# Performance work log

Hardware: AMD Instinct MI355X
Metric: run time of the kernel (lower is better)

Reference implementation:

```python
import jax, jax.numpy as jnp
import numpy as np


def gcn_conv(x, src, dst, W, b, n_nodes):
    # PyG GCNConv default: add self-loops, symmetric normalization D^-1/2 A D^-1/2.
    h = x @ W  # [N, out]
    # degree with unit edge weights + self loop
    deg = jnp.zeros((n_nodes,), dtype=x.dtype).at[dst].add(1.0) + 1.0
    dinv = jax.lax.rsqrt(deg)  # deg >= 1, safe
    norm = dinv[src] * dinv[dst]  # [E]
    msg = h[src] * norm[:, None]  # [E, out] gather + scale
    out = jnp.zeros_like(h).at[dst].add(msg)  # scatter-add aggregate
    # self-loop contribution: norm_ii = dinv_i^2
    out = out + h * (dinv * dinv)[:, None]
    return out + b


def setup_inputs() -> dict:
    key = jax.random.key(0)
    ks = jax.random.split(key, 10)
    N, E, F_in, H, G = 100000, 1600000, 128, 128, 256
    x = jax.random.normal(ks[0], (N, F_in), dtype=jnp.float32)
    edge_index = jax.random.randint(ks[1], (2, E), 0, N, dtype=jnp.int64)
    batch = jnp.sort(jax.random.randint(ks[2], (N,), 0, G, dtype=jnp.int64))
    s1 = 1.0 / np.sqrt(F_in)
    s2 = 1.0 / np.sqrt(H)
    W1 = jax.random.uniform(ks[3], (F_in, H), jnp.float32, -s1, s1)
    b1 = jnp.zeros((H,), jnp.float32)
    W2 = jax.random.uniform(ks[4], (H, H), jnp.float32, -s2, s2)
    b2 = jnp.zeros((H,), jnp.float32)
    Wlin = jax.random.uniform(ks[5], (H, 2), jnp.float32, -s2, s2)
    blin = jax.random.uniform(ks[6], (2,), jnp.float32, -s2, s2)
    return {"x": x, "edge_index": edge_index, "batch": batch, "num_graphs": G,
            "W1": W1, "b1": b1, "W2": W2, "b2": b2, "Wlin": Wlin, "blin": blin}


def reference(x, edge_index, batch, num_graphs, W1, b1, W2, b2, Wlin, blin):
    n_nodes = x.shape[0]
    src, dst = edge_index[0], edge_index[1]
    h = jax.nn.relu(gcn_conv(x, src, dst, W1, b1, n_nodes))
    h = jax.nn.relu(gcn_conv(h, src, dst, W2, b2, n_nodes))
    # global_mean_pool over graphs
    sums = jax.ops.segment_sum(h, batch, num_segments=num_graphs)
    counts = jax.ops.segment_sum(jnp.ones((n_nodes,), h.dtype), batch, num_segments=num_graphs)
    pooled = sums / jnp.maximum(counts, 1.0)[:, None]  # [G, H]
    return pooled @ Wlin + blin  # [G, 2]
```

## Files before the change

### kernel.cpp

```cpp
#include <hip/hip_runtime.h>
#include <hip/hip_bf16.h>


#define FEAT 128
#define GRAPHS 256
#define CH 2048
#define BSH 8
#define MAXNB 512

typedef short bf16x8 __attribute__((ext_vector_type(8)));
typedef float f32x4 __attribute__((ext_vector_type(4)));

__device__ inline unsigned bf16rne(float f) {
    unsigned u = __float_as_uint(f);
    return (u + 0x7FFFu + ((u >> 16) & 1u)) >> 16;
}

#define SWZ(row, kbyte) ((kbyte) ^ (((row) & 7) << 4))

__global__ __launch_bounds__(256) void kb_hist(const int* __restrict__ dst, int E, int NB,
                                               int* __restrict__ bhist) {
    __shared__ int h[MAXNB];
    for (int i = threadIdx.x; i < NB; i += 256) h[i] = 0;
    __syncthreads();
    int stride = gridDim.x * 256;
    for (int i = blockIdx.x * 256 + threadIdx.x; i < E; i += stride)
        atomicAdd(&h[dst[i] >> BSH], 1);
    __syncthreads();
    for (int i = threadIdx.x; i < NB; i += 256)
        if (h[i]) atomicAdd(&bhist[i], h[i]);
}

__global__ void kb_scan(const int* __restrict__ bhist, int NB,
                        int* __restrict__ bbase, int* __restrict__ bcur) {
    __shared__ int s[512];
    int t = threadIdx.x;
    int v = (t < NB) ? bhist[t] : 0;
    s[t] = v;
    __syncthreads();
    for (int d = 1; d < 512; d <<= 1) {
        int a = (t >= d) ? s[t - d] : 0;
        __syncthreads();
        s[t] += a;
        __syncthreads();
    }
    if (t < NB) { int e = s[t] - v; bbase[t] = e; bcur[t] = e; }
}

__global__ __launch_bounds__(256) void kb_group(const int* __restrict__ src,
                                                const int* __restrict__ dst, int E, int NB,
                                                int* __restrict__ bcur,
                                                unsigned* __restrict__ stg) {
    __shared__ int lhist[MAXNB], lcur[MAXNB], gdelta[MAXNB], sc[512];
    __shared__ unsigned lpak[CH];
    __shared__ int gp[CH];
    int t = threadIdx.x;
    int base = blockIdx.x * CH;
    int n = E - base; if (n > CH) n = CH;

    for (int i = t; i < NB; i += 256) lhist[i] = 0;
    __syncthreads();

    unsigned pk[8]; int bk[8]; int nl = 0;
#pragma unroll
    for (int j = 0; j < 8; ++j) {
        int k = j * 256 + t;
        if (k < n) {
            int d = dst[base + k];
            int sv = src[base + k];
            int b = d >> BSH;
            pk[nl] = ((unsigned)(d & ((1 << BSH) - 1)) << 17) | (unsigned)sv;
            bk[nl] = b; nl++;
            atomicAdd(&lhist[b], 1);
        }
    }
    __syncthreads();

    for (int i = t; i < 512; i += 256) sc[i] = (i < NB) ? lhist[i] : 0;
    __syncthreads();
    for (int d = 1; d < 512; d <<= 1) {
        int a0 = (t >= d) ? sc[t - d] : 0;
        int a1 = sc[t + 256 - d];
        __syncthreads();
        sc[t] += a0; sc[t + 256] += a1;
        __syncthreads();
    }
    for (int i = t; i < NB; i += 256) {
        int c = lhist[i];
        int lb = sc[i] - c;
        lcur[i] = lb;
        int g = c ? atomicAdd(&bcur[i], c) : 0;
        gdelta[i] = g - lb;
    }
    __syncthreads();

    for (int j = 0; j < nl; ++j) {
        int b = bk[j];
        int slot = atomicAdd(&lcur[b], 1);
        lpak[slot] = pk[j];
        gp[slot] = gdelta[b] + slot;
    }
    __syncthreads();
    for (int i = t; i < n; i += 256) stg[gp[i]] = lpak[i];
}

__global__ __launch_bounds__(256) void kb_csr(const unsigned* __restrict__ stg,
                                              const int* __restrict__ bbase,
                                              const int* __restrict__ bhist, int N,
                                              int* __restrict__ ssrc, int* __restrict__ off,
                                              int* __restrict__ cnt, float* __restrict__ dinv) {
    __shared__ int h[256], lcur[256], sc[256];
    int b = blockIdx.x;
    int t = threadIdx.x;
    int s0 = bbase[b], m = bhist[b];
    h[t] = 0;
    __syncthreads();
    for (int i = t; i < m; i += 256) atomicAdd(&h[stg[s0 + i] >> 17], 1);
    __syncthreads();
    int v = h[t];
    sc[t] = v;
    __syncthreads();
    for (int d = 1; d < 256; d <<= 1) {
        int a = (t >= d) ? sc[t - d] : 0;
        __syncthreads();
        sc[t] += a;
        __syncthreads();
    }
    int lb = sc[t] - v;
    lcur[t] = lb;
    int node = (b << BSH) + t;
    if (node < N) {
        off[node] = s0 + lb;
        cnt[node] = v;
        dinv[node] = rsqrtf(1.0f + (float)v);
    }
    __syncthreads();
    for (int i = t; i < m; i += 256) {
        unsigned p = stg[s0 + i];
        int d = p >> 17;
        int r = atomicAdd(&lcur[d], 1);
        ssrc[s0 + r] = (int)(p & 0x1FFFFu);
    }
}

__global__ void k_gstart(const int* __restrict__ batch, int N, int G, int* __restrict__ gstart) {
    int i = blockIdx.x * blockDim.x + threadIdx.x;
    if (i >= N) return;
    int b = batch[i];
    int bp = (i == 0) ? -1 : batch[i - 1];
    for (int g = bp + 1; g <= b; ++g) gstart[g] = i;
    if (i == N - 1) {
        for (int g = b + 1; g <= G; ++g) gstart[g] = N;
    }
}

__global__ void k_wpre(const float* __restrict__ W, unsigned short* __restrict__ Wpre) {
    int tid = blockIdx.x * 256 + threadIdx.x;
    int frag = tid >> 6;
    int l = tid & 63;
    int cf = frag >> 2, ks = frag & 3;
    int col = cf * 16 + (l & 15);
    int k0 = ks * 32 + (l >> 4) * 8;
    unsigned short o[8];
#pragma unroll
    for (int j = 0; j < 8; ++j)
        o[j] = (unsigned short)bf16rne(W[(k0 + j) * 128 + col]);
    *(uint4*)(Wpre + (size_t)tid * 8) = *(const uint4*)o;
}

__device__ inline unsigned umax16pair(unsigned d, unsigned cur) {
    unsigned a = d & 0x7FFF7FFFu;
    unsigned lo = a & 0xFFFFu, hi = a >> 16;
    unsigned m = lo > hi ? lo : hi;
    return m > cur ? m : cur;
}
__device__ inline unsigned q8b(float x, float si) {
    return (unsigned)(__float2int_rn(x * si) + 128) & 0xFFu;
}
__device__ inline unsigned pack2(unsigned d0, unsigned d1, float si) {
    float x0 = __uint_as_float(d0 << 16);
    float x1 = __uint_as_float(d0 & 0xFFFF0000u);
    float x2 = __uint_as_float(d1 << 16);
    float x3 = __uint_as_float(d1 & 0xFFFF0000u);
    return q8b(x0, si) | (q8b(x1, si) << 8) | (q8b(x2, si) << 16) | (q8b(x3, si) << 24);
}

template <bool BF16IN>
__global__ __launch_bounds__(256, 4) void k_gemm_mfma(const void* __restrict__ Xv,
                                                      const unsigned short* __restrict__ Wpre,
                                                      const float* __restrict__ dinv,
                                                      unsigned char* __restrict__ Q8,
                                                      float* __restrict__ srow, int N) {
    __shared__ __align__(16) unsigned short sA[128 * 128];
    __shared__ unsigned sMaxH[256];
    int t = threadIdx.x;
    int r0 = blockIdx.x * 128;
    int rows = N - r0; if (rows > 128) rows = 128;

    if constexpr (!BF16IN) {
        const float4* X4 = (const float4*)((const float*)Xv + (size_t)r0 * 128);
#pragma unroll
        for (int j = 0; j < 16; ++j) {
            int f = j * 256 + t;
            int row = f >> 5, q = f & 31;
            float4 v = make_float4(0.f, 0.f, 0.f, 0.f);
            if (row < rows) v = X4[f];
            unsigned lo = bf16rne(v.x) | (bf16rne(v.y) << 16);
            unsigned hi = bf16rne(v.z) | (bf16rne(v.w) << 16);
            int byte = row * 256 + SWZ(row, q * 8);
            *(uint2*)((char*)sA + byte) = make_uint2(lo, hi);
        }
    } else {
        const uint4* X4 = (const uint4*)((const unsigned short*)Xv + (size_t)r0 * 128);
#pragma unroll
        for (int j = 0; j < 8; ++j) {
            int f = j * 256 + t;
            int row = f >> 4, q = f & 15;
            uint4 v = make_uint4(0u, 0u, 0u, 0u);
            if (row < rows) v = X4[f];
            int byte = row * 256 + SWZ(row, q * 16);
            *(uint4*)((char*)sA + byte) = v;
        }
    }
    __syncthreads();

    int w = t >> 6, l = t & 63;
    int wr = (w >> 1) * 64, wc = (w & 1) * 64;
    int lr = l & 15, kc = l >> 4;

    f32x4 acc[4][4] = {};
    for (int ks = 0; ks < 4; ++ks) {
        bf16x8 a[4], b[4];
#pragma unroll
        for (int m = 0; m < 4; ++m) {
            int row = wr + m * 16 + lr;
            int byte = row * 256 + SWZ(row, ks * 64 + kc * 16);
            a[m] = *(const bf16x8*)((const char*)sA + byte);
        }
#pragma unroll
        for (int n = 0; n < 4; ++n) {
            int cf = (wc >> 4) + n;
            b[n] = *(const bf16x8*)(Wpre + ((size_t)((cf * 4 + ks) * 64 + l) * 8));
        }
#pragma unroll
        for (int m = 0; m < 4; ++m)
#pragma unroll
            for (int n = 0; n < 4; ++n)
                acc[m][n] = __builtin_amdgcn_mfma_f32_16x16x32_bf16(a[m], b[n], acc[m][n], 0, 0, 0);
    }
    __syncthreads();

#pragma unroll
    for (int m = 0; m < 4; ++m) {
        int rbase = wr + m * 16 + kc * 4;
#pragma unroll
        for (int r = 0; r < 4; ++r) {
            int row = rbase + r;
            float dv = (r0 + row < N) ? dinv[r0 + row] : 0.f;
#pragma unroll
            for (int n = 0; n < 4; ++n) {
                int col = wc + n * 16 + lr;
                sA[row * 128 + col] = (unsigned short)bf16rne(acc[m][n][r] * dv);
            }
        }
    }
    __syncthreads();

    {
        int r = t >> 1, hh = t & 1;
        const uint4* rowp = (const uint4*)(sA + r * 128 + hh * 64);
        uint4 wreg[8];
#pragma unroll
        for (int j = 0; j < 8; ++j) wreg[j] = rowp[j];
        unsigned mb = 0;
#pragma unroll
        for (int j = 0; j < 8; ++j) {
            mb = umax16pair(wreg[j].x, mb);
            mb = umax16pair(wreg[j].y, mb);
            mb = umax16pair(wreg[j].z, mb);
            mb = umax16pair(wreg[j].w, mb);
        }
        sMaxH[r * 2 + hh] = mb;
        __syncthreads();
        unsigned m0 = sMaxH[r * 2], m1 = sMaxH[r * 2 + 1];
        unsigned m16 = m0 > m1 ? m0 : m1;
        float mv = __uint_as_float(m16 << 16);
        float si = (mv > 0.f) ? 127.0f / mv : 0.0f;
        if (hh == 0 && r0 + r < N) srow[r0 + r] = mv * (1.0f / 127.0f);
        if (r0 + r < N) {
            unsigned q[16];
#pragma unroll
            for (int j = 0; j < 8; ++j) {
                q[2 * j]     = pack2(wreg[j].x, wreg[j].y, si);
                q[2 * j + 1] = pack2(wreg[j].z, wreg[j].w, si);
            }
            uint4* qo = (uint4*)(Q8 + (size_t)(r0 + r) * 128 + hh * 64);
            qo[0] = make_uint4(q[0], q[1], q[2], q[3]);
            qo[1] = make_uint4(q[4], q[5], q[6], q[7]);
            qo[2] = make_uint4(q[8], q[9], q[10], q[11]);
            qo[3] = make_uint4(q[12], q[13], q[14], q[15]);
        }
    }
}

#define ACC8(d, sc) { float _s = (sc);                       \
    a0 += _s * (float)((d) & 0xFFu);                         \
    a1 += _s * (float)(((d) >> 8) & 0xFFu);                  \
    a2 += _s * (float)(((d) >> 16) & 0xFFu);                 \
    a3 += _s * (float)((d) >> 24);                           \
    ssum += _s; }

__global__ __launch_bounds__(256) void k_agg8(const unsigned char* __restrict__ Q8,
                                              const float* __restrict__ srow,
                                              const int* __restrict__ off,
                                              const int* __restrict__ cnt,
                                              const int* __restrict__ ssrc,
                                              const float* __restrict__ dinv,
                                              const float* __restrict__ b,
                                              unsigned* __restrict__ OUTB, int N) {
    int wid = (blockIdx.x * blockDim.x + threadIdx.x) >> 6;
    if (wid >= N) return;
    int l = threadIdx.x & 63;
    int half = l >> 5, c4 = l & 31;
    int v = wid;
    int s = off[v], c = cnt[v];
    int K = (c + 1) >> 1;
    int ib = s + (half ? K : 0);
    int ie = half ? (s + c) : (s + K);

    float a0 = 0.f, a1 = 0.f, a2 = 0.f, a3 = 0.f, ssum = 0.f;
    if (!half) {
        unsigned d = *(const unsigned*)(Q8 + (size_t)v * 128 + c4 * 4);
        float sc = srow[v];
        ACC8(d, sc)
    }
    while (ib + 8 <= ie) {
        int u0 = ssrc[ib],     u1 = ssrc[ib + 1], u2 = ssrc[ib + 2], u3 = ssrc[ib + 3];
        int u4 = ssrc[ib + 4], u5 = ssrc[ib + 5], u6 = ssrc[ib + 6], u7 = ssrc[ib + 7];
        unsigned d0 = *(const unsigned*)(Q8 + (size_t)u0 * 128 + c4 * 4);
        unsigned d1 = *(const unsigned*)(Q8 + (size_t)u1 * 128 + c4 * 4);
        unsigned d2 = *(const unsigned*)(Q8 + (size_t)u2 * 128 + c4 * 4);
        unsigned d3 = *(const unsigned*)(Q8 + (size_t)u3 * 128 + c4 * 4);
        unsigned d4 = *(const unsigned*)(Q8 + (size_t)u4 * 128 + c4 * 4);
        unsigned d5 = *(const unsigned*)(Q8 + (size_t)u5 * 128 + c4 * 4);
        unsigned d6 = *(const unsigned*)(Q8 + (size_t)u6 * 128 + c4 * 4);
        unsigned d7 = *(const unsigned*)(Q8 + (size_t)u7 * 128 + c4 * 4);
        float s0 = srow[u0], s1 = srow[u1], s2 = srow[u2], s3 = srow[u3];
        float s4 = srow[u4], s5 = srow[u5], s6 = srow[u6], s7 = srow[u7];
        ACC8(d0, s0) ACC8(d1, s1) ACC8(d2, s2) ACC8(d3, s3)
        ACC8(d4, s4) ACC8(d5, s5) ACC8(d6, s6) ACC8(d7, s7)
        ib += 8;
    }
    while (ib < ie) {
        int u = ssrc[ib++];
        unsigned d = *(const unsigned*)(Q8 + (size_t)u * 128 + c4 * 4);
        float sc = srow[u];
        ACC8(d, sc)
    }
    a0 += __shfl_xor(a0, 32);
    a1 += __shfl_xor(a1, 32);
    a2 += __shfl_xor(a2, 32);
    a3 += __shfl_xor(a3, 32);
    ssum += __shfl_xor(ssum, 32);
    if (!half) {
        float dv = dinv[v];
        float4 bb = *(const float4*)(b + c4 * 4);
        float o0 = fmaxf((a0 - 128.f * ssum) * dv + bb.x, 0.f);
        float o1 = fmaxf((a1 - 128.f * ssum) * dv + bb.y, 0.f);
        float o2 = fmaxf((a2 - 128.f * ssum) * dv + bb.z, 0.f);
        float o3 = fmaxf((a3 - 128.f * ssum) * dv + bb.w, 0.f);
        uint2 wv;
        wv.x = bf16rne(o0) | (bf16rne(o1) << 16);
        wv.y = bf16rne(o2) | (bf16rne(o3) << 16);
        ((uint2*)(OUTB + (size_t)v * 64))[c4] = wv;
    }
}

__global__ __launch_bounds__(256) void k_pool_head(const unsigned* __restrict__ H2,
                                                   const int* __restrict__ gstart,
                                                   const float* __restrict__ Wlin,
                                                   const float* __restrict__ blin,
                                                   float* __restrict__ out, int G) {
    __shared__ float2 stmp[256];
    __shared__ float sp[128];
    int g = blockIdx.x;
    int t = threadIdx.x;
    int p = t & 63, quarter = t >> 6;
    int s = gstart[g], e = gstart[g + 1];
    float2 acc = make_float2(0.f, 0.f);
    for (int i = s + quarter; i < e; i += 4) {
        unsigned u = H2[(size_t)i * 64 + p];
        acc.x += __uint_as_float(u << 16);
        acc.y += __uint_as_float(u & 0xFFFF0000u);
    }
    stmp[t] = acc;
    __syncthreads();
    if (t < 64) {
        float2 a = stmp[t];
        a.x += stmp[t + 64].x + stmp[t + 128].x + stmp[t + 192].x;
        a.y += stmp[t + 64].y + stmp[t + 128].y + stmp[t + 192].y;
        float inv = 1.0f / fmaxf((float)(e - s), 1.0f);
        sp[2 * t] = a.x * inv;
        sp[2 * t + 1] = a.y * inv;
    }
    __syncthreads();
    if (t < 2) {
        float a = 0.0f;
        for (int j = 0; j < 128; ++j) a += sp[j] * Wlin[j * 2 + t];
        out[g * 2 + t] = a + blin[t];
    }
}

extern "C" void kernel_launch(void* const* d_in, const int* in_sizes, int n_in,
                              void* d_out, int out_size, void* d_ws, size_t ws_size,
                              hipStream_t stream) {
    const float* x     = (const float*)d_in[0];
    const int*   ei    = (const int*)d_in[1];
    const int*   batch = (const int*)d_in[2];
    const float* W1    = (const float*)d_in[4];
    const float* b1    = (const float*)d_in[5];
    const float* W2    = (const float*)d_in[6];
    const float* b2    = (const float*)d_in[7];
    const float* Wlin  = (const float*)d_in[8];
    const float* blin  = (const float*)d_in[9];
    float* out = (float*)d_out;

    const int N = in_sizes[0] / FEAT;
    const int E = in_sizes[1] / 2;
    const int G = GRAPHS;
    const int NB = (N + (1 << BSH) - 1) >> BSH;
    const int* src = ei;
    const int* dst = ei + E;

    char* ws = (char*)d_ws;
    unsigned char* q8 = (unsigned char*)ws;
    float* srow = (float*)(q8 + (size_t)N * FEAT);
    unsigned short* hact = (unsigned short*)(srow + N);
    int*   ssrc = (int*)(hact + (size_t)N * FEAT);
    unsigned* stg = (unsigned*)(ssrc + E);
    int*   off  = (int*)(stg + E);
    int*   cnt  = off + N;
    float* dinv = (float*)(cnt + N);
    int*   bhist = (int*)(dinv + N);
    int*   bbase = bhist + MAXNB;
    int*   bcur  = bbase + MAXNB;
    int*   gstart = bcur + MAXNB;
    unsigned short* wpre1 = (unsigned short*)(gstart + G + 2);
    unsigned short* wpre2 = wpre1 + 16384;

    const int nb = (N + 255) / 256;
    const int nch = (E + CH - 1) / CH;
    const int ngb = (N + 127) / 128;

    hipMemsetAsync(bhist, 0, (size_t)NB * sizeof(int), stream);

    k_wpre<<<8, 256, 0, stream>>>(W1, wpre1);
    k_wpre<<<8, 256, 0, stream>>>(W2, wpre2);

    kb_hist<<<256, 256, 0, stream>>>(dst, E, NB, bhist);
    kb_scan<<<1, 512, 0, stream>>>(bhist, NB, bbase, bcur);
    kb_group<<<nch, 256, 0, stream>>>(src, dst, E, NB, bcur, stg);
    kb_csr<<<NB, 256, 0, stream>>>(stg, bbase, bhist, N, ssrc, off, cnt, dinv);

    k_gstart<<<nb, 256, 0, stream>>>(batch, N, G, gstart);

    k_gemm_mfma<false><<<ngb, 256, 0, stream>>>(x, wpre1, dinv, q8, srow, N);
    k_agg8<<<(N + 3) / 4, 256, 0, stream>>>(q8, srow, off, cnt, ssrc, dinv, b1, (unsigned*)hact, N);
    k_gemm_mfma<true><<<ngb, 256, 0, stream>>>(hact, wpre2, dinv, q8, srow, N);
    k_agg8<<<(N + 3) / 4, 256, 0, stream>>>(q8, srow, off, cnt, ssrc, dinv, b2, (unsigned*)hact, N);

    k_pool_head<<<G, 256, 0, stream>>>((const unsigned*)hact, gstart, Wlin, blin, out, G);
}
```

Before: 383.5 us.

## Aggregate each node with 8 lanes using wide loads and degree-sorted node order

The gather-aggregate kernel now assigns 8 lanes per destination node instead of a full 64-lane wavefront. Each lane loads 16 bytes of the int8 row and keeps 16 accumulators, and neighbour indices are read four at a time with an int4 load. Three small kernels (histogram, scan, scatter) build a permutation that groups nodes by clamped degree, so the 8 nodes sharing a wavefront have similar loop lengths. This aims to raise memory-level parallelism and cut idle lanes on low-degree nodes. The cost is extra preprocessing launches, more registers per lane, permuted output writes, and possibly misaligned int4 index loads.

```diff
diff --git a/kernel.cpp b/kernel.cpp
--- a/kernel.cpp
+++ b/kernel.cpp
@@ -15,6 +15,8 @@
     unsigned u = __float_as_uint(f);
     return (u + 0x7FFFu + ((u >> 16) & 1u)) >> 16;
 }
+__device__ inline float bfl(unsigned u) { return __uint_as_float(u << 16); }
+__device__ inline float bfh(unsigned u) { return __uint_as_float(u & 0xFFFF0000u); }
 
 #define SWZ(row, kbyte) ((kbyte) ^ (((row) & 7) << 4))
 
@@ -143,6 +145,33 @@
     }
 }
 
+__global__ void k_dhist(const int* __restrict__ cnt, int N, int* __restrict__ dh) {
+    int i = blockIdx.x * blockDim.x + threadIdx.x;
+    if (i < N) atomicAdd(&dh[min(cnt[i], 63)], 1);
+}
+__global__ void k_dscan(const int* __restrict__ dh, int* __restrict__ dcur) {
+    __shared__ int s[64];
+    int t = threadIdx.x;
+    int v = dh[t];
+    s[t] = v;
+    __syncthreads();
+    for (int d = 1; d < 64; d <<= 1) {
+        int a = (t >= d) ? s[t - d] : 0;
+        __syncthreads();
+        s[t] += a;
+        __syncthreads();
+    }
+    dcur[t] = s[t] - v;
+}
+__global__ void k_dperm(const int* __restrict__ cnt, int N, int* __restrict__ dcur,
+                        int* __restrict__ perm) {
+    int i = blockIdx.x * blockDim.x + threadIdx.x;
+    if (i < N) {
+        int p = atomicAdd(&dcur[min(cnt[i], 63)], 1);
+        perm[p] = i;
+    }
+}
+
 __global__ void k_gstart(const int* __restrict__ batch, int N, int G, int* __restrict__ gstart) {
     int i = blockIdx.x * blockDim.x + threadIdx.x;
     if (i >= N) return;
@@ -178,10 +207,7 @@
     return (unsigned)(__float2int_rn(x * si) + 128) & 0xFFu;
 }
 __device__ inline unsigned pack2(unsigned d0, unsigned d1, float si) {
-    float x0 = __uint_as_float(d0 << 16);
-    float x1 = __uint_as_float(d0 & 0xFFFF0000u);
-    float x2 = __uint_as_float(d1 << 16);
-    float x3 = __uint_as_float(d1 & 0xFFFF0000u);
+    float x0 = bfl(d0), x1 = bfh(d0), x2 = bfl(d1), x3 = bfh(d1);
     return q8b(x0, si) | (q8b(x1, si) << 8) | (q8b(x2, si) << 16) | (q8b(x3, si) << 24);
 }
 
@@ -303,77 +329,90 @@
     }
 }
 
-#define ACC8(d, sc) { float _s = (sc);                       \
-    a0 += _s * (float)((d) & 0xFFu);                         \
-    a1 += _s * (float)(((d) >> 8) & 0xFFu);                  \
-    a2 += _s * (float)(((d) >> 16) & 0xFFu);                 \
-    a3 += _s * (float)((d) >> 24);                           \
-    ssum += _s; }
+#define ACCU(u, s, A, B, C, D) {                      \
+    A = fmaf(s, (float)((u) & 0xFFu), A);             \
+    B = fmaf(s, (float)(((u) >> 8) & 0xFFu), B);      \
+    C = fmaf(s, (float)(((u) >> 16) & 0xFFu), C);     \
+    D = fmaf(s, (float)((u) >> 24), D); }
+#define ACCROW8(R, S) { float _s = (S); ssum += _s;   \
+    ACCU(R.x, _s, a0, a1, a2, a3)                     \
+    ACCU(R.y, _s, a4, a5, a6, a7)                     \
+    ACCU(R.z, _s, a8, a9, a10, a11)                   \
+    ACCU(R.w, _s, a12, a13, a14, a15) }
 
 __global__ __launch_bounds__(256) void k_agg8(const unsigned char* __restrict__ Q8,
                                               const float* __restrict__ srow,
                                               const int* __restrict__ off,
                                               const int* __restrict__ cnt,
                                               const int* __restrict__ ssrc,
+                                              const int* __restrict__ perm,
                                               const float* __restrict__ dinv,
                                               const float* __restrict__ b,
                                               unsigned* __restrict__ OUTB, int N) {
-    int wid = (blockIdx.x * blockDim.x + threadIdx.x) >> 6;
-    if (wid >= N) return;
-    int l = threadIdx.x & 63;
-    int half = l >> 5, c4 = l & 31;
-    int v = wid;
-    int s = off[v], c = cnt[v];
-    int K = (c + 1) >> 1;
-    int ib = s + (half ? K : 0);
-    int ie = half ? (s + c) : (s + K);
-
-    float a0 = 0.f, a1 = 0.f, a2 = 0.f, a3 = 0.f, ssum = 0.f;
-    if (!half) {
-        unsigned d = *(const unsigned*)(Q8 + (size_t)v * 128 + c4 * 4);
-        float sc = srow[v];
-        ACC8(d, sc)
-    }
-    while (ib + 8 <= ie) {
-        int u0 = ssrc[ib],     u1 = ssrc[ib + 1], u2 = ssrc[ib + 2], u3 = ssrc[ib + 3];
-        int u4 = ssrc[ib + 4], u5 = ssrc[ib + 5], u6 = ssrc[ib + 6], u7 = ssrc[ib + 7];
-        unsigned d0 = *(const unsigned*)(Q8 + (size_t)u0 * 128 + c4 * 4);
-        unsigned d1 = *(const unsigned*)(Q8 + (size_t)u1 * 128 + c4 * 4);
-        unsigned d2 = *(const unsigned*)(Q8 + (size_t)u2 * 128 + c4 * 4);
-        unsigned d3 = *(const unsigned*)(Q8 + (size_t)u3 * 128 + c4 * 4);
-        unsigned d4 = *(const unsigned*)(Q8 + (size_t)u4 * 128 + c4 * 4);
-        unsigned d5 = *(const unsigned*)(Q8 + (size_t)u5 * 128 + c4 * 4);
-        unsigned d6 = *(const unsigned*)(Q8 + (size_t)u6 * 128 + c4 * 4);
-        unsigned d7 = *(const unsigned*)(Q8 + (size_t)u7 * 128 + c4 * 4);
-        float s0 = srow[u0], s1 = srow[u1], s2 = srow[u2], s3 = srow[u3];
-        float s4 = srow[u4], s5 = srow[u5], s6 = srow[u6], s7 = srow[u7];
-        ACC8(d0, s0) ACC8(d1, s1) ACC8(d2, s2) ACC8(d3, s3)
-        ACC8(d4, s4) ACC8(d5, s5) ACC8(d6, s6) ACC8(d7, s7)
-        ib += 8;
-    }
-    while (ib < ie) {
-        int u = ssrc[ib++];
-        unsigned d = *(const unsigned*)(Q8 + (size_t)u * 128 + c4 * 4);
-        float sc = srow[u];
-        ACC8(d, sc)
-    }
-    a0 += __shfl_xor(a0, 32);
-    a1 += __shfl_xor(a1, 32);
-    a2 += __shfl_xor(a2, 32);
-    a3 += __shfl_xor(a3, 32);
-    ssum += __shfl_xor(ssum, 32);
-    if (!half) {
-        float dv = dinv[v];
-        float4 bb = *(const float4*)(b + c4 * 4);
-        float o0 = fmaxf((a0 - 128.f * ssum) * dv + bb.x, 0.f);
-        float o1 = fmaxf((a1 - 128.f * ssum) * dv + bb.y, 0.f);
-        float o2 = fmaxf((a2 - 128.f * ssum) * dv + bb.z, 0.f);
-        float o3 = fmaxf((a3 - 128.f * ssum) * dv + bb.w, 0.f);
-        uint2 wv;
-        wv.x = bf16rne(o0) | (bf16rne(o1) << 16);
-        wv.y = bf16rne(o2) | (bf16rne(o3) << 16);
-        ((uint2*)(OUTB + (size_t)v * 64))[c4] = wv;
-    }
+    int slot = (blockIdx.x * blockDim.x + threadIdx.x) >> 3;
+    if (slot >= N) return;
+    int j = threadIdx.x & 7;
+    int v = perm[slot];
+
+    float a0 = 0.f, a1 = 0.f, a2 = 0.f, a3 = 0.f, a4 = 0.f, a5 = 0.f, a6 = 0.f, a7 = 0.f;
+    float a8 = 0.f, a9 = 0.f, a10 = 0.f, a11 = 0.f, a12 = 0.f, a13 = 0.f, a14 = 0.f, a15 = 0.f;
+    float ssum = 0.f;
+
+    {
+        uint4 r = *(const uint4*)(Q8 + (size_t)v * 128 + j * 16);
+        float s = srow[v];
+        ACCROW8(r, s)
+    }
+    int i = off[v], e = i + cnt[v];
+    for (; i + 4 <= e; i += 4) {
+        int4 uu = *(const int4*)(ssrc + i);
+        uint4 r0 = *(const uint4*)(Q8 + (size_t)uu.x * 128 + j * 16);
+        uint4 r1 = *(const uint4*)(Q8 + (size_t)uu.y * 128 + j * 16);
+        uint4 r2 = *(const uint4*)(Q8 + (size_t)uu.z * 128 + j * 16);
+        uint4 r3 = *(const uint4*)(Q8 + (size_t)uu.w * 128 + j * 16);
+        float s0 = srow[uu.x], s1 = srow[uu.y], s2 = srow[uu.z], s3 = srow[uu.w];
+        ACCROW8(r0, s0) ACCROW8(r1, s1) ACCROW8(r2, s2) ACCROW8(r3, s3)
+    }
+    for (; i < e; ++i) {
+        int u = ssrc[i];
+        uint4 r = *(const uint4*)(Q8 + (size_t)u * 128 + j * 16);
+        float s = srow[u];
+        ACCROW8(r, s)
+    }
+
+    float dv = dinv[v];
+    float corr = 128.f * ssum;
+    const float4* B4 = (const float4*)(b + j * 16);
+    float4 bb0 = B4[0], bb1 = B4[1], bb2 = B4[2], bb3 = B4[3];
+    float o0  = fmaxf((a0  - corr) * dv + bb0.x, 0.f);
+    float o1  = fmaxf((a1  - corr) * dv + bb0.y, 0.f);
+    float o2  = fmaxf((a2  - corr) * dv + bb0.z, 0.f);
+    float o3  = fmaxf((a3  - corr) * dv + bb0.w, 0.f);
+    float o4  = fmaxf((a4  - corr) * dv + bb1.x, 0.f);
+    float o5  = fmaxf((a5  - corr) * dv + bb1.y, 0.f);
+    float o6  = fmaxf((a6  - corr) * dv + bb1.z, 0.f);
+    float o7  = fmaxf((a7  - corr) * dv + bb1.w, 0.f);
+    float o8  = fmaxf((a8  - corr) * dv + bb2.x, 0.f);
+    float o9  = fmaxf((a9  - corr) * dv + bb2.y, 0.f);
+    float o10 = fmaxf((a10 - corr) * dv + bb2.z, 0.f);
+    float o11 = fmaxf((a11 - corr) * dv + bb2.w, 0.f);
+    float o12 = fmaxf((a12 - corr) * dv + bb3.x, 0.f);
+    float o13 = fmaxf((a13 - corr) * dv + bb3.y, 0.f);
+    float o14 = fmaxf((a14 - corr) * dv + bb3.z, 0.f);
+    float o15 = fmaxf((a15 - corr) * dv + bb3.w, 0.f);
+
+    uint4 w0, w1;
+    w0.x = bf16rne(o0)  | (bf16rne(o1)  << 16);
+    w0.y = bf16rne(o2)  | (bf16rne(o3)  << 16);
+    w0.z = bf16rne(o4)  | (bf16rne(o5)  << 16);
+    w0.w = bf16rne(o6)  | (bf16rne(o7)  << 16);
+    w1.x = bf16rne(o8)  | (bf16rne(o9)  << 16);
+    w1.y = bf16rne(o10) | (bf16rne(o11) << 16);
+    w1.z = bf16rne(o12) | (bf16rne(o13) << 16);
+    w1.w = bf16rne(o14) | (bf16rne(o15) << 16);
+    uint4* orow = (uint4*)OUTB + (size_t)v * 16 + j * 2;
+    orow[0] = w0;
+    orow[1] = w1;
 }
 
 __global__ __launch_bounds__(256) void k_pool_head(const unsigned* __restrict__ H2,
@@ -390,8 +429,8 @@
     float2 acc = make_float2(0.f, 0.f);
     for (int i = s + quarter; i < e; i += 4) {
         unsigned u = H2[(size_t)i * 64 + p];
-        acc.x += __uint_as_float(u << 16);
-        acc.y += __uint_as_float(u & 0xFFFF0000u);
+        acc.x += bfl(u);
+        acc.y += bfh(u);
     }
     stmp[t] = acc;
     __syncthreads();
@@ -441,10 +480,13 @@
     int*   off  = (int*)(stg + E);
     int*   cnt  = off + N;
     float* dinv = (float*)(cnt + N);
-    int*   bhist = (int*)(dinv + N);
+    int*   perm = (int*)(dinv + N);
+    int*   bhist = perm + N;
     int*   bbase = bhist + MAXNB;
     int*   bcur  = bbase + MAXNB;
-    int*   gstart = bcur + MAXNB;
+    int*   dh    = bcur + MAXNB;
+    int*   dcur  = dh + 64;
+    int*   gstart = dcur + 64;
     unsigned short* wpre1 = (unsigned short*)(gstart + G + 2);
     unsigned short* wpre2 = wpre1 + 16384;
 
@@ -453,6 +495,7 @@
     const int ngb = (N + 127) / 128;
 
     hipMemsetAsync(bhist, 0, (size_t)NB * sizeof(int), stream);
+    hipMemsetAsync(dh, 0, 64 * sizeof(int), stream);
 
     k_wpre<<<8, 256, 0, stream>>>(W1, wpre1);
     k_wpre<<<8, 256, 0, stream>>>(W2, wpre2);
@@ -462,12 +505,16 @@
     kb_group<<<nch, 256, 0, stream>>>(src, dst, E, NB, bcur, stg);
     kb_csr<<<NB, 256, 0, stream>>>(stg, bbase, bhist, N, ssrc, off, cnt, dinv);
 
+    k_dhist<<<nb, 256, 0, stream>>>(cnt, N, dh);
+    k_dscan<<<1, 64, 0, stream>>>(dh, dcur);
+    k_dperm<<<nb, 256, 0, stream>>>(cnt, N, dcur, perm);
+
     k_gstart<<<nb, 256, 0, stream>>>(batch, N, G, gstart);
 
     k_gemm_mfma<false><<<ngb, 256, 0, stream>>>(x, wpre1, dinv, q8, srow, N);
-    k_agg8<<<(N + 3) / 4, 256, 0, stream>>>(q8, srow, off, cnt, ssrc, dinv, b1, (unsigned*)hact, N);
+    k_agg8<<<(N * 8 + 255) / 256, 256, 0, stream>>>(q8, srow, off, cnt, ssrc, perm, dinv, b1, (unsigned*)hact, N);
     k_gemm_mfma<true><<<ngb, 256, 0, stream>>>(hact, wpre2, dinv, q8, srow, N);
-    k_agg8<<<(N + 3) / 4, 256, 0, stream>>>(q8, srow, off, cnt, ssrc, dinv, b2, (unsigned*)hact, N);
+    k_agg8<<<(N * 8 + 255) / 256, 256, 0, stream>>>(q8, srow, off, cnt, ssrc, perm, dinv, b2, (unsigned*)hact, N);
 
     k_pool_head<<<G, 256, 0, stream>>>((const unsigned*)hact, gstart, Wlin, blin, out, G);
 }
```

Result: slower. 846.5 us (+120.7%).
